# Kernel tuning notes

Hardware: AMD Instinct MI355X
Metric: run time of the kernel (lower is better)

## Reference

```python
import jax, jax.numpy as jnp
import numpy as np

B, T, D, H, HD, FF = 1024, 128, 128, 4, 32, 512
SCALE = D ** -0.5  # NOTE: original scales by full EMBED_DIM**-0.5, not head_dim
EPS = 1e-5


def setup_inputs() -> dict:
    key = jax.random.key(0)
    ks = jax.random.split(key, 14)
    s = 0.02
    return {
        "x": jax.random.normal(ks[0], (B, T, D), dtype=jnp.float32),
        "ln1_g": jnp.ones((D,), jnp.float32),
        "ln1_b": jnp.zeros((D,), jnp.float32),
        "Wq": jax.random.normal(ks[1], (H, HD, D), jnp.float32) * s,
        "Wk": jax.random.normal(ks[2], (H, HD, D), jnp.float32) * s,
        "Wv": jax.random.normal(ks[3], (H, HD, D), jnp.float32) * s,
        "Wo": jax.random.normal(ks[4], (D, D), jnp.float32) * s,
        "bo": jnp.zeros((D,), jnp.float32),
        "ln2_g": jnp.ones((D,), jnp.float32),
        "ln2_b": jnp.zeros((D,), jnp.float32),
        "W1": jax.random.normal(ks[5], (FF, D), jnp.float32) * s,
        "b1": jnp.zeros((FF,), jnp.float32),
        "W2": jax.random.normal(ks[6], (D, FF), jnp.float32) * s,
        "b2": jnp.zeros((D,), jnp.float32),
    }


def _layer_norm(x, g, b):
    mu = jnp.mean(x, axis=-1, keepdims=True)
    var = jnp.mean(jnp.square(x - mu), axis=-1, keepdims=True)
    return (x - mu) * jax.lax.rsqrt(var + EPS) * g + b


def reference(x, ln1_g, ln1_b, Wq, Wk, Wv, Wo, bo, ln2_g, ln2_b, W1, b1, W2, b2):
    # --- attention sub-block ---
    h = _layer_norm(x, ln1_g, ln1_b)                       # [B,T,D]
    q = jnp.einsum('btd,nhd->bnth', h, Wq)                 # [B,H,T,HD]
    k = jnp.einsum('btd,nhd->bnth', h, Wk)
    v = jnp.einsum('btd,nhd->bnth', h, Wv)
    scores = jnp.einsum('bnth,bnsh->bnts', q, k) * SCALE   # [B,H,T,T]
    causal = jnp.tril(jnp.ones((T, T), dtype=bool))
    scores = jnp.where(causal, scores, -jnp.inf)
    w = jax.nn.softmax(scores, axis=-1)                    # dropout = eval identity
    attn = jnp.einsum('bnts,bnsh->bnth', w, v)             # [B,H,T,HD]
    attn = attn.transpose(0, 2, 1, 3).reshape(B, T, D)     # concat heads
    x = x + attn @ Wo.T + bo
    # --- feed-forward sub-block ---
    h2 = _layer_norm(x, ln2_g, ln2_b)
    ff = jax.nn.relu(h2 @ W1.T + b1) @ W2.T + b2
    return x + ff
```

## Files before the change

kernel.cpp:

```cpp
#include <hip/hip_runtime.h>
#include <hip/hip_bf16.h>


typedef short bf16x8 __attribute__((ext_vector_type(8)));
typedef float f32x4  __attribute__((ext_vector_type(4)));
typedef unsigned short u16;
typedef unsigned int   u32;

#define TT   128
#define DDIM 128
#define FFD  512
#define PIT  136

__device__ __forceinline__ u16 f2b(float f) {
    __hip_bfloat16 h = __float2bfloat16(f);
    return __builtin_bit_cast(u16, h);
}
__device__ __forceinline__ bf16x8 ldfrag(const u16* p) {
    return __builtin_bit_cast(bf16x8, *reinterpret_cast<const uint4*>(p));
}
__device__ __forceinline__ bf16x8 ldfrag_f32(const float* p) {
    float4 a = *reinterpret_cast<const float4*>(p);
    float4 b = *reinterpret_cast<const float4*>(p + 4);
    bf16x8 r;
    r[0] = (short)f2b(a.x); r[1] = (short)f2b(a.y);
    r[2] = (short)f2b(a.z); r[3] = (short)f2b(a.w);
    r[4] = (short)f2b(b.x); r[5] = (short)f2b(b.y);
    r[6] = (short)f2b(b.z); r[7] = (short)f2b(b.w);
    return r;
}
__device__ __forceinline__ f32x4 mfma16(bf16x8 a, bf16x8 b, f32x4 c) {
    return __builtin_amdgcn_mfma_f32_16x16x32_bf16(a, b, c, 0, 0, 0);
}

__global__ __launch_bounds__(512, 2) void tblock_kernel(
    const float* __restrict__ x,
    const float* __restrict__ ln1g, const float* __restrict__ ln1b,
    const float* __restrict__ Wq,   const float* __restrict__ Wk, const float* __restrict__ Wv,
    const float* __restrict__ Wo,   const float* __restrict__ bo,
    const float* __restrict__ ln2g, const float* __restrict__ ln2b,
    const float* __restrict__ W1,   const float* __restrict__ b1,
    const float* __restrict__ W2,   const float* __restrict__ b2,
    float* __restrict__ out)
{
    __shared__ __align__(16) u16 sm[4 * TT * PIT];
    u16* bufA = sm;
    u16* bufB = sm + 1 * TT * PIT;
    u16* bufC = sm + 2 * TT * PIT;
    u16* bufD = sm + 3 * TT * PIT;

    const int b    = blockIdx.x;
    const int tid  = threadIdx.x;
    const int w    = tid >> 6;
    const int l    = tid & 63;
    const int lq   = l & 15;
    const int quad = l >> 4;
    const float* xb = x + (size_t)b * (TT * DDIM);

    {
        const int row = tid >> 2, part = tid & 3;
        const float* src = xb + row * DDIM + part * 32;
        float v[32];
        float s = 0.f, s2 = 0.f;
        #pragma unroll
        for (int i = 0; i < 8; i++) {
            float4 u = *reinterpret_cast<const float4*>(src + i * 4);
            v[i * 4 + 0] = u.x; v[i * 4 + 1] = u.y;
            v[i * 4 + 2] = u.z; v[i * 4 + 3] = u.w;
            s  += u.x + u.y + u.z + u.w;
            s2 += u.x * u.x + u.y * u.y + u.z * u.z + u.w * u.w;
        }
        s  += __shfl_xor(s, 1);  s2 += __shfl_xor(s2, 1);
        s  += __shfl_xor(s, 2);  s2 += __shfl_xor(s2, 2);
        float mean = s * (1.f / 128.f);
        float var  = fmaxf(s2 * (1.f / 128.f) - mean * mean, 0.f);
        float rstd = rsqrtf(var + 1e-5f);
        u16* dst = bufA + row * PIT + part * 32;
        #pragma unroll
        for (int i = 0; i < 4; i++) {
            u32 o4[4];
            #pragma unroll
            for (int j = 0; j < 4; j++) {
                int c = part * 32 + i * 8 + 2 * j;
                float r0 = (v[i * 8 + 2 * j]     - mean) * rstd * ln1g[c]     + ln1b[c];
                float r1 = (v[i * 8 + 2 * j + 1] - mean) * rstd * ln1g[c + 1] + ln1b[c + 1];
                o4[j] = (u32)f2b(r0) | ((u32)f2b(r1) << 16);
            }
            uint4 pk; pk.x = o4[0]; pk.y = o4[1]; pk.z = o4[2]; pk.w = o4[3];
            *reinterpret_cast<uint4*>(dst + i * 8) = pk;
        }
    }
    __syncthreads();

    {
        bf16x8 bq[4], bk[4];
        #pragma unroll
        for (int ks = 0; ks < 4; ks++) {
            bq[ks] = ldfrag_f32(Wq + (w * 16 + lq) * DDIM + ks * 32 + quad * 8);
            bk[ks] = ldfrag_f32(Wk + (w * 16 + lq) * DDIM + ks * 32 + quad * 8);
        }
        #pragma unroll
        for (int m = 0; m < 8; m++) {
            f32x4 accq = {0, 0, 0, 0}, acck = {0, 0, 0, 0};
            #pragma unroll
            for (int ks = 0; ks < 4; ks++) {
                bf16x8 a = ldfrag(bufA + (m * 16 + lq) * PIT + ks * 32 + quad * 8);
                accq = mfma16(a, bq[ks], accq);
                acck = mfma16(a, bk[ks], acck);
            }
            #pragma unroll
            for (int r = 0; r < 4; r++) {
                int t = m * 16 + quad * 4 + r;
                bufB[t * PIT + w * 16 + lq] = f2b(accq[r]);
                bufC[t * PIT + w * 16 + lq] = f2b(acck[r]);
            }
        }
        bf16x8 av[4];
        #pragma unroll
        for (int ks = 0; ks < 4; ks++)
            av[ks] = ldfrag_f32(Wv + (w * 16 + lq) * DDIM + ks * 32 + quad * 8);
        #pragma unroll
        for (int n = 0; n < 8; n++) {
            f32x4 acc = {0, 0, 0, 0};
            #pragma unroll
            for (int ks = 0; ks < 4; ks++) {
                bf16x8 bh = ldfrag(bufA + (n * 16 + lq) * PIT + ks * 32 + quad * 8);
                acc = mfma16(av[ks], bh, acc);
            }
            #pragma unroll
            for (int r = 0; r < 4; r++) {
                int o = w * 16 + quad * 4 + r;
                bufD[o * PIT + n * 16 + lq] = f2b(acc[r]);
            }
        }
    }
    __syncthreads();

    const float SCALE = 0.08838834764831845f;
    #pragma unroll 1
    for (int h = 0; h < 4; h++) {
        bf16x8 aq = ldfrag(bufB + (w * 16 + lq) * PIT + h * 32 + quad * 8);
        float p[8][4];
        #pragma unroll
        for (int n = 0; n < 8; n++) {
            bf16x8 bk = ldfrag(bufC + (n * 16 + lq) * PIT + h * 32 + quad * 8);
            f32x4 s4 = {0, 0, 0, 0};
            s4 = mfma16(aq, bk, s4);
            #pragma unroll
            for (int r = 0; r < 4; r++) p[n][r] = s4[r];
        }
        #pragma unroll
        for (int r = 0; r < 4; r++) {
            int t = w * 16 + quad * 4 + r;
            float mx = -3.0e38f;
            #pragma unroll
            for (int n = 0; n < 8; n++) {
                int sc = n * 16 + lq;
                float val = p[n][r] * SCALE;
                p[n][r] = val;
                mx = (sc <= t) ? fmaxf(mx, val) : mx;
            }
            mx = fmaxf(mx, __shfl_xor(mx, 1));
            mx = fmaxf(mx, __shfl_xor(mx, 2));
            mx = fmaxf(mx, __shfl_xor(mx, 4));
            mx = fmaxf(mx, __shfl_xor(mx, 8));
            float sum = 0.f;
            #pragma unroll
            for (int n = 0; n < 8; n++) {
                int sc = n * 16 + lq;
                float e = (sc <= t) ? __expf(p[n][r] - mx) : 0.f;
                p[n][r] = e; sum += e;
            }
            sum += __shfl_xor(sum, 1);
            sum += __shfl_xor(sum, 2);
            sum += __shfl_xor(sum, 4);
            sum += __shfl_xor(sum, 8);
            float inv = 1.f / sum;
            #pragma unroll
            for (int n = 0; n < 8; n++)
                bufA[t * PIT + n * 16 + lq] = f2b(p[n][r] * inv);
        }
        __syncthreads();
        f32x4 o0 = {0, 0, 0, 0}, o1 = {0, 0, 0, 0};
        #pragma unroll
        for (int ks = 0; ks < 4; ks++) {
            bf16x8 ap  = ldfrag(bufA + (w * 16 + lq) * PIT + ks * 32 + quad * 8);
            bf16x8 bv0 = ldfrag(bufD + (h * 32 + lq) * PIT + ks * 32 + quad * 8);
            bf16x8 bv1 = ldfrag(bufD + (h * 32 + 16 + lq) * PIT + ks * 32 + quad * 8);
            o0 = mfma16(ap, bv0, o0);
            o1 = mfma16(ap, bv1, o1);
        }
        __syncthreads();
        #pragma unroll
        for (int r = 0; r < 4; r++) {
            int t = w * 16 + quad * 4 + r;
            bufB[t * PIT + h * 32 + lq]      = f2b(o0[r]);
            bufB[t * PIT + h * 32 + 16 + lq] = f2b(o1[r]);
        }
    }
    __syncthreads();

    float x1res[8][4];
    const int dcol = w * 16 + lq;
    {
        bf16x8 bw[4];
        #pragma unroll
        for (int ks = 0; ks < 4; ks++)
            bw[ks] = ldfrag_f32(Wo + (w * 16 + lq) * DDIM + ks * 32 + quad * 8);
        const float bov = bo[dcol];
        #pragma unroll
        for (int m = 0; m < 8; m++) {
            f32x4 acc = {0, 0, 0, 0};
            #pragma unroll
            for (int ks = 0; ks < 4; ks++) {
                bf16x8 a = ldfrag(bufB + (m * 16 + lq) * PIT + ks * 32 + quad * 8);
                acc = mfma16(a, bw[ks], acc);
            }
            #pragma unroll
            for (int r = 0; r < 4; r++) {
                int t = m * 16 + quad * 4 + r;
                float xv = xb[t * DDIM + dcol];
                float x1 = acc[r] + xv + bov;
                x1res[m][r] = x1;
                bufC[t * PIT + dcol] = f2b(x1);
            }
        }
    }
    __syncthreads();

    {
        const int row = tid >> 2, part = tid & 3;
        const u16* src = bufC + row * PIT + part * 32;
        float v[32];
        float s = 0.f, s2 = 0.f;
        #pragma unroll
        for (int i = 0; i < 4; i++) {
            uint4 u = *reinterpret_cast<const uint4*>(src + i * 8);
            u32 arr[4] = {u.x, u.y, u.z, u.w};
            #pragma unroll
            for (int j = 0; j < 4; j++) {
                float f0 = __uint_as_float((arr[j] & 0xffffu) << 16);
                float f1 = __uint_as_float(arr[j] & 0xffff0000u);
                v[i * 8 + 2 * j] = f0; v[i * 8 + 2 * j + 1] = f1;
                s += f0 + f1; s2 += f0 * f0 + f1 * f1;
            }
        }
        s  += __shfl_xor(s, 1);  s2 += __shfl_xor(s2, 1);
        s  += __shfl_xor(s, 2);  s2 += __shfl_xor(s2, 2);
        float mean = s * (1.f / 128.f);
        float var  = fmaxf(s2 * (1.f / 128.f) - mean * mean, 0.f);
        float rstd = rsqrtf(var + 1e-5f);
        u16* dst = bufD + row * PIT + part * 32;
        #pragma unroll
        for (int i = 0; i < 4; i++) {
            u32 o4[4];
            #pragma unroll
            for (int j = 0; j < 4; j++) {
                int c = part * 32 + i * 8 + 2 * j;
                float r0 = (v[i * 8 + 2 * j]     - mean) * rstd * ln2g[c]     + ln2b[c];
                float r1 = (v[i * 8 + 2 * j + 1] - mean) * rstd * ln2g[c + 1] + ln2b[c + 1];
                o4[j] = (u32)f2b(r0) | ((u32)f2b(r1) << 16);
            }
            uint4 pk; pk.x = o4[0]; pk.y = o4[1]; pk.z = o4[2]; pk.w = o4[3];
            *reinterpret_cast<uint4*>(dst + i * 8) = pk;
        }
    }
    __syncthreads();

    f32x4 oacc[8];
    #pragma unroll
    for (int m = 0; m < 8; m++) oacc[m] = f32x4{0, 0, 0, 0};

    #pragma unroll 1
    for (int fc = 0; fc < 4; fc++) {
        const int fbase = fc * 128;
        bf16x8 wf1[4];
        #pragma unroll
        for (int ks = 0; ks < 4; ks++)
            wf1[ks] = ldfrag_f32(W1 + (fbase + w * 16 + lq) * DDIM + ks * 32 + quad * 8);
        const float b1v = b1[fbase + w * 16 + lq];
        #pragma unroll
        for (int m = 0; m < 8; m++) {
            f32x4 acc = {0, 0, 0, 0};
            #pragma unroll
            for (int ks = 0; ks < 4; ks++) {
                bf16x8 a = ldfrag(bufD + (m * 16 + lq) * PIT + ks * 32 + quad * 8);
                acc = mfma16(a, wf1[ks], acc);
            }
            #pragma unroll
            for (int r = 0; r < 4; r++) {
                int t = m * 16 + quad * 4 + r;
                float g = acc[r] + b1v;
                g = g > 0.f ? g : 0.f;
                bufA[t * PIT + w * 16 + lq] = f2b(g);
            }
        }
        __syncthreads();
        bf16x8 wf2[4];
        #pragma unroll
        for (int ks = 0; ks < 4; ks++)
            wf2[ks] = ldfrag_f32(W2 + (w * 16 + lq) * FFD + fbase + ks * 32 + quad * 8);
        #pragma unroll
        for (int m = 0; m < 8; m++) {
            #pragma unroll
            for (int ks = 0; ks < 4; ks++) {
                bf16x8 a = ldfrag(bufA + (m * 16 + lq) * PIT + ks * 32 + quad * 8);
                oacc[m] = mfma16(a, wf2[ks], oacc[m]);
            }
        }
        __syncthreads();
    }

    {
        const float b2v = b2[dcol];
        float* ob = out + (size_t)b * (TT * DDIM);
        #pragma unroll
        for (int m = 0; m < 8; m++) {
            #pragma unroll
            for (int r = 0; r < 4; r++) {
                int t = m * 16 + quad * 4 + r;
                ob[t * DDIM + dcol] = oacc[m][r] + x1res[m][r] + b2v;
            }
        }
    }
}

extern "C" void kernel_launch(void* const* d_in, const int* in_sizes, int n_in,
                              void* d_out, int out_size, void* d_ws, size_t ws_size,
                              hipStream_t stream) {
    const float* x    = (const float*)d_in[0];
    const float* ln1g = (const float*)d_in[1];
    const float* ln1b = (const float*)d_in[2];
    const float* Wq   = (const float*)d_in[3];
    const float* Wk   = (const float*)d_in[4];
    const float* Wv   = (const float*)d_in[5];
    const float* Wo   = (const float*)d_in[6];
    const float* bo   = (const float*)d_in[7];
    const float* ln2g = (const float*)d_in[8];
    const float* ln2b = (const float*)d_in[9];
    const float* W1   = (const float*)d_in[10];
    const float* b1   = (const float*)d_in[11];
    const float* W2   = (const float*)d_in[12];
    const float* b2   = (const float*)d_in[13];
    float* out = (float*)d_out;

    const int nblocks = in_sizes[0] / (TT * DDIM);
    tblock_kernel<<<dim3(nblocks), dim3(512), 0, stream>>>(
        x, ln1g, ln1b, Wq, Wk, Wv, Wo, bo, ln2g, ln2b, W1, b1, W2, b2, out);
}
```

Measured before the change: 323.3 us.

## Compute QKV per head, fuse Wo per head, and shrink LDS for higher occupancy

Attention is restructured so Q, K and V are computed one head at a time into small per-head LDS buffers, and the Wo projection is accumulated per head in registers. Shared memory drops from four 128x136 buffers to about 74KB, which allows the launch bound to target 4 blocks per CU instead of 2. It also skips causally masked score and PV tiles using the wave-uniform wave index. In exchange there are more barriers per head and more reloads of the weights from global memory, and register pressure rises under the tighter launch bound.

Result: slower. 448.4 us (+38.7%).

```diff
diff --git a/kernel.cpp b/kernel.cpp
--- a/kernel.cpp
+++ b/kernel.cpp
@@ -11,6 +11,7 @@
 #define DDIM 128
 #define FFD  512
 #define PIT  136
+#define QPIT 40
 
 __device__ __forceinline__ u16 f2b(float f) {
     __hip_bfloat16 h = __float2bfloat16(f);
@@ -33,7 +34,7 @@
     return __builtin_amdgcn_mfma_f32_16x16x32_bf16(a, b, c, 0, 0, 0);
 }
 
-__global__ __launch_bounds__(512, 2) void tblock_kernel(
+__global__ __launch_bounds__(512, 4) void tblock_kernel(
     const float* __restrict__ x,
     const float* __restrict__ ln1g, const float* __restrict__ ln1b,
     const float* __restrict__ Wq,   const float* __restrict__ Wk, const float* __restrict__ Wv,
@@ -43,11 +44,13 @@
     const float* __restrict__ W2,   const float* __restrict__ b2,
     float* __restrict__ out)
 {
-    __shared__ __align__(16) u16 sm[4 * TT * PIT];
-    u16* bufA = sm;
-    u16* bufB = sm + 1 * TT * PIT;
-    u16* bufC = sm + 2 * TT * PIT;
-    u16* bufD = sm + 3 * TT * PIT;
+    __shared__ __align__(16) u16 sm[37120];
+    u16* hs  = sm;
+    u16* Qh  = sm + 17408;
+    u16* Kh  = sm + 22528;
+    u16* Vth = sm + 27648;
+    u16* Pst = sm + 32000;
+    u16* h2b = sm + 17408;
 
     const int b    = blockIdx.x;
     const int tid  = threadIdx.x;
@@ -55,7 +58,9 @@
     const int l    = tid & 63;
     const int lq   = l & 15;
     const int quad = l >> 4;
+    const int wu   = __builtin_amdgcn_readfirstlane(w);
     const float* xb = x + (size_t)b * (TT * DDIM);
+    const int dcol = w * 16 + lq;
 
     {
         const int row = tid >> 2, part = tid & 3;
@@ -75,7 +80,7 @@
         float mean = s * (1.f / 128.f);
         float var  = fmaxf(s2 * (1.f / 128.f) - mean * mean, 0.f);
         float rstd = rsqrtf(var + 1e-5f);
-        u16* dst = bufA + row * PIT + part * 32;
+        u16* dst = hs + row * PIT + part * 32;
         #pragma unroll
         for (int i = 0; i < 4; i++) {
             u32 o4[4];
@@ -92,137 +97,148 @@
     }
     __syncthreads();
 
-    {
-        bf16x8 bq[4], bk[4];
-        #pragma unroll
-        for (int ks = 0; ks < 4; ks++) {
-            bq[ks] = ldfrag_f32(Wq + (w * 16 + lq) * DDIM + ks * 32 + quad * 8);
-            bk[ks] = ldfrag_f32(Wk + (w * 16 + lq) * DDIM + ks * 32 + quad * 8);
-        }
-        #pragma unroll
-        for (int m = 0; m < 8; m++) {
-            f32x4 accq = {0, 0, 0, 0}, acck = {0, 0, 0, 0};
-            #pragma unroll
-            for (int ks = 0; ks < 4; ks++) {
-                bf16x8 a = ldfrag(bufA + (m * 16 + lq) * PIT + ks * 32 + quad * 8);
-                accq = mfma16(a, bq[ks], accq);
-                acck = mfma16(a, bk[ks], acck);
-            }
-            #pragma unroll
-            for (int r = 0; r < 4; r++) {
-                int t = m * 16 + quad * 4 + r;
-                bufB[t * PIT + w * 16 + lq] = f2b(accq[r]);
-                bufC[t * PIT + w * 16 + lq] = f2b(acck[r]);
-            }
-        }
-        bf16x8 av[4];
-        #pragma unroll
-        for (int ks = 0; ks < 4; ks++)
-            av[ks] = ldfrag_f32(Wv + (w * 16 + lq) * DDIM + ks * 32 + quad * 8);
-        #pragma unroll
-        for (int n = 0; n < 8; n++) {
-            f32x4 acc = {0, 0, 0, 0};
-            #pragma unroll
-            for (int ks = 0; ks < 4; ks++) {
-                bf16x8 bh = ldfrag(bufA + (n * 16 + lq) * PIT + ks * 32 + quad * 8);
-                acc = mfma16(av[ks], bh, acc);
-            }
-            #pragma unroll
-            for (int r = 0; r < 4; r++) {
-                int o = w * 16 + quad * 4 + r;
-                bufD[o * PIT + n * 16 + lq] = f2b(acc[r]);
-            }
-        }
-    }
-    __syncthreads();
-
     const float SCALE = 0.08838834764831845f;
+    f32x4 x1a[8];
+    #pragma unroll
+    for (int m = 0; m < 8; m++) x1a[m] = f32x4{0, 0, 0, 0};
+
     #pragma unroll 1
     for (int h = 0; h < 4; h++) {
-        bf16x8 aq = ldfrag(bufB + (w * 16 + lq) * PIT + h * 32 + quad * 8);
-        float p[8][4];
-        #pragma unroll
-        for (int n = 0; n < 8; n++) {
-            bf16x8 bk = ldfrag(bufC + (n * 16 + lq) * PIT + h * 32 + quad * 8);
-            f32x4 s4 = {0, 0, 0, 0};
-            s4 = mfma16(aq, bk, s4);
-            #pragma unroll
-            for (int r = 0; r < 4; r++) p[n][r] = s4[r];
-        }
-        #pragma unroll
-        for (int r = 0; r < 4; r++) {
-            int t = w * 16 + quad * 4 + r;
-            float mx = -3.0e38f;
+        {
+            const float* WqB = Wq + (size_t)(h * 32) * DDIM;
+            const float* WkB = Wk + (size_t)(h * 32) * DDIM;
+            #pragma unroll
+            for (int nt = 0; nt < 2; nt++) {
+                f32x4 aq = {0, 0, 0, 0}, ak = {0, 0, 0, 0};
+                #pragma unroll
+                for (int ks = 0; ks < 4; ks++) {
+                    bf16x8 a  = ldfrag(hs + (w * 16 + lq) * PIT + ks * 32 + quad * 8);
+                    bf16x8 bq = ldfrag_f32(WqB + (nt * 16 + lq) * DDIM + ks * 32 + quad * 8);
+                    bf16x8 bk = ldfrag_f32(WkB + (nt * 16 + lq) * DDIM + ks * 32 + quad * 8);
+                    aq = mfma16(a, bq, aq);
+                    ak = mfma16(a, bk, ak);
+                }
+                #pragma unroll
+                for (int r = 0; r < 4; r++) {
+                    int t = w * 16 + quad * 4 + r;
+                    Qh[t * QPIT + nt * 16 + lq] = f2b(aq[r]);
+                    Kh[t * QPIT + nt * 16 + lq] = f2b(ak[r]);
+                }
+            }
+            const float* WvB = Wv + (size_t)(h * 32) * DDIM;
+            #pragma unroll
+            for (int mt = 0; mt < 2; mt++) {
+                f32x4 av = {0, 0, 0, 0};
+                #pragma unroll
+                for (int ks = 0; ks < 4; ks++) {
+                    bf16x8 a  = ldfrag_f32(WvB + (mt * 16 + lq) * DDIM + ks * 32 + quad * 8);
+                    bf16x8 bh = ldfrag(hs + (w * 16 + lq) * PIT + ks * 32 + quad * 8);
+                    av = mfma16(a, bh, av);
+                }
+                #pragma unroll
+                for (int r = 0; r < 4; r++) {
+                    int o = mt * 16 + quad * 4 + r;
+                    Vth[o * PIT + w * 16 + lq] = f2b(av[r]);
+                }
+            }
+        }
+        __syncthreads();
+
+        {
+            bf16x8 aq = ldfrag(Qh + (w * 16 + lq) * QPIT + quad * 8);
+            float p[8][4];
+            #pragma unroll
+            for (int n = 0; n < 8; n++)
+                #pragma unroll
+                for (int r = 0; r < 4; r++) p[n][r] = 0.f;
             #pragma unroll
             for (int n = 0; n < 8; n++) {
-                int sc = n * 16 + lq;
-                float val = p[n][r] * SCALE;
-                p[n][r] = val;
-                mx = (sc <= t) ? fmaxf(mx, val) : mx;
-            }
-            mx = fmaxf(mx, __shfl_xor(mx, 1));
-            mx = fmaxf(mx, __shfl_xor(mx, 2));
-            mx = fmaxf(mx, __shfl_xor(mx, 4));
-            mx = fmaxf(mx, __shfl_xor(mx, 8));
-            float sum = 0.f;
-            #pragma unroll
-            for (int n = 0; n < 8; n++) {
-                int sc = n * 16 + lq;
-                float e = (sc <= t) ? __expf(p[n][r] - mx) : 0.f;
-                p[n][r] = e; sum += e;
-            }
-            sum += __shfl_xor(sum, 1);
-            sum += __shfl_xor(sum, 2);
-            sum += __shfl_xor(sum, 4);
-            sum += __shfl_xor(sum, 8);
-            float inv = 1.f / sum;
-            #pragma unroll
-            for (int n = 0; n < 8; n++)
-                bufA[t * PIT + n * 16 + lq] = f2b(p[n][r] * inv);
+                if (n <= wu) {
+                    bf16x8 bk = ldfrag(Kh + (n * 16 + lq) * QPIT + quad * 8);
+                    f32x4 s4 = {0, 0, 0, 0};
+                    s4 = mfma16(aq, bk, s4);
+                    #pragma unroll
+                    for (int r = 0; r < 4; r++) p[n][r] = s4[r];
+                }
+            }
+            #pragma unroll
+            for (int r = 0; r < 4; r++) {
+                int t = w * 16 + quad * 4 + r;
+                float mx = -3.0e38f;
+                #pragma unroll
+                for (int n = 0; n < 8; n++) {
+                    int sc = n * 16 + lq;
+                    float val = p[n][r] * SCALE;
+                    p[n][r] = val;
+                    mx = (sc <= t) ? fmaxf(mx, val) : mx;
+                }
+                mx = fmaxf(mx, __shfl_xor(mx, 1));
+                mx = fmaxf(mx, __shfl_xor(mx, 2));
+                mx = fmaxf(mx, __shfl_xor(mx, 4));
+                mx = fmaxf(mx, __shfl_xor(mx, 8));
+                float sum = 0.f;
+                #pragma unroll
+                for (int n = 0; n < 8; n++) {
+                    int sc = n * 16 + lq;
+                    float e = (sc <= t) ? __expf(p[n][r] - mx) : 0.f;
+                    p[n][r] = e; sum += e;
+                }
+                sum += __shfl_xor(sum, 1);
+                sum += __shfl_xor(sum, 2);
+                sum += __shfl_xor(sum, 4);
+                sum += __shfl_xor(sum, 8);
+                float inv = 1.f / sum;
+                #pragma unroll
+                for (int n = 0; n < 8; n++) p[n][r] *= inv;
+            }
+            f32x4 o0 = {0, 0, 0, 0}, o1 = {0, 0, 0, 0};
+            #pragma unroll
+            for (int s = 0; s < 4; s++) {
+                if (s <= (wu >> 1)) {
+                    #pragma unroll
+                    for (int r = 0; r < 4; r++) {
+                        int t = w * 16 + quad * 4 + r;
+                        Pst[t * QPIT + lq]      = f2b(p[2 * s][r]);
+                        Pst[t * QPIT + 16 + lq] = f2b(p[2 * s + 1][r]);
+                    }
+                    bf16x8 ap  = ldfrag(Pst + (w * 16 + lq) * QPIT + quad * 8);
+                    bf16x8 bv0 = ldfrag(Vth + lq * PIT        + s * 32 + quad * 8);
+                    bf16x8 bv1 = ldfrag(Vth + (16 + lq) * PIT + s * 32 + quad * 8);
+                    o0 = mfma16(ap, bv0, o0);
+                    o1 = mfma16(ap, bv1, o1);
+                }
+            }
+            #pragma unroll
+            for (int r = 0; r < 4; r++) {
+                int t = w * 16 + quad * 4 + r;
+                Qh[t * QPIT + lq]      = f2b(o0[r]);
+                Qh[t * QPIT + 16 + lq] = f2b(o1[r]);
+            }
         }
         __syncthreads();
-        f32x4 o0 = {0, 0, 0, 0}, o1 = {0, 0, 0, 0};
-        #pragma unroll
-        for (int ks = 0; ks < 4; ks++) {
-            bf16x8 ap  = ldfrag(bufA + (w * 16 + lq) * PIT + ks * 32 + quad * 8);
-            bf16x8 bv0 = ldfrag(bufD + (h * 32 + lq) * PIT + ks * 32 + quad * 8);
-            bf16x8 bv1 = ldfrag(bufD + (h * 32 + 16 + lq) * PIT + ks * 32 + quad * 8);
-            o0 = mfma16(ap, bv0, o0);
-            o1 = mfma16(ap, bv1, o1);
-        }
-        __syncthreads();
-        #pragma unroll
-        for (int r = 0; r < 4; r++) {
-            int t = w * 16 + quad * 4 + r;
-            bufB[t * PIT + h * 32 + lq]      = f2b(o0[r]);
-            bufB[t * PIT + h * 32 + 16 + lq] = f2b(o1[r]);
-        }
-    }
-    __syncthreads();
-
-    float x1res[8][4];
-    const int dcol = w * 16 + lq;
+
+        {
+            bf16x8 bwo = ldfrag_f32(Wo + (size_t)(w * 16 + lq) * DDIM + h * 32 + quad * 8);
+            #pragma unroll
+            for (int m = 0; m < 8; m++) {
+                bf16x8 a = ldfrag(Qh + (m * 16 + lq) * QPIT + quad * 8);
+                x1a[m] = mfma16(a, bwo, x1a[m]);
+            }
+        }
+        if (h < 3) __syncthreads();
+    }
+
     {
-        bf16x8 bw[4];
-        #pragma unroll
-        for (int ks = 0; ks < 4; ks++)
-            bw[ks] = ldfrag_f32(Wo + (w * 16 + lq) * DDIM + ks * 32 + quad * 8);
         const float bov = bo[dcol];
         #pragma unroll
         for (int m = 0; m < 8; m++) {
-            f32x4 acc = {0, 0, 0, 0};
-            #pragma unroll
-            for (int ks = 0; ks < 4; ks++) {
-                bf16x8 a = ldfrag(bufB + (m * 16 + lq) * PIT + ks * 32 + quad * 8);
-                acc = mfma16(a, bw[ks], acc);
-            }
             #pragma unroll
             for (int r = 0; r < 4; r++) {
                 int t = m * 16 + quad * 4 + r;
                 float xv = xb[t * DDIM + dcol];
-                float x1 = acc[r] + xv + bov;
-                x1res[m][r] = x1;
-                bufC[t * PIT + dcol] = f2b(x1);
+                float v = x1a[m][r] + xv + bov;
+                x1a[m][r] = v;
+                hs[t * PIT + dcol] = f2b(v);
             }
         }
     }
@@ -230,7 +246,7 @@
 
     {
         const int row = tid >> 2, part = tid & 3;
-        const u16* src = bufC + row * PIT + part * 32;
+        const u16* src = hs + row * PIT + part * 32;
         float v[32];
         float s = 0.f, s2 = 0.f;
         #pragma unroll
@@ -250,7 +266,7 @@
         float mean = s * (1.f / 128.f);
         float var  = fmaxf(s2 * (1.f / 128.f) - mean * mean, 0.f);
         float rstd = rsqrtf(var + 1e-5f);
-        u16* dst = bufD + row * PIT + part * 32;
+        u16* dst = h2b + row * PIT + part * 32;
         #pragma unroll
         for (int i = 0; i < 4; i++) {
             u32 o4[4];
@@ -270,6 +286,7 @@
     f32x4 oacc[8];
     #pragma unroll
     for (int m = 0; m < 8; m++) oacc[m] = f32x4{0, 0, 0, 0};
+    u16* Gb = hs;
 
     #pragma unroll 1
     for (int fc = 0; fc < 4; fc++) {
@@ -277,14 +294,14 @@
         bf16x8 wf1[4];
         #pragma unroll
         for (int ks = 0; ks < 4; ks++)
-            wf1[ks] = ldfrag_f32(W1 + (fbase + w * 16 + lq) * DDIM + ks * 32 + quad * 8);
+            wf1[ks] = ldfrag_f32(W1 + (size_t)(fbase + w * 16 + lq) * DDIM + ks * 32 + quad * 8);
         const float b1v = b1[fbase + w * 16 + lq];
         #pragma unroll
         for (int m = 0; m < 8; m++) {
             f32x4 acc = {0, 0, 0, 0};
             #pragma unroll
             for (int ks = 0; ks < 4; ks++) {
-                bf16x8 a = ldfrag(bufD + (m * 16 + lq) * PIT + ks * 32 + quad * 8);
+                bf16x8 a = ldfrag(h2b + (m * 16 + lq) * PIT + ks * 32 + quad * 8);
                 acc = mfma16(a, wf1[ks], acc);
             }
             #pragma unroll
@@ -292,19 +309,19 @@
                 int t = m * 16 + quad * 4 + r;
                 float g = acc[r] + b1v;
                 g = g > 0.f ? g : 0.f;
-                bufA[t * PIT + w * 16 + lq] = f2b(g);
+                Gb[t * PIT + w * 16 + lq] = f2b(g);
             }
         }
         __syncthreads();
         bf16x8 wf2[4];
         #pragma unroll
         for (int ks = 0; ks < 4; ks++)
-            wf2[ks] = ldfrag_f32(W2 + (w * 16 + lq) * FFD + fbase + ks * 32 + quad * 8);
+            wf2[ks] = ldfrag_f32(W2 + (size_t)(w * 16 + lq) * FFD + fbase + ks * 32 + quad * 8);
         #pragma unroll
         for (int m = 0; m < 8; m++) {
             #pragma unroll
             for (int ks = 0; ks < 4; ks++) {
-                bf16x8 a = ldfrag(bufA + (m * 16 + lq) * PIT + ks * 32 + quad * 8);
+                bf16x8 a = ldfrag(Gb + (m * 16 + lq) * PIT + ks * 32 + quad * 8);
                 oacc[m] = mfma16(a, wf2[ks], oacc[m]);
             }
         }
@@ -319,7 +336,7 @@
             #pragma unroll
             for (int r = 0; r < 4; r++) {
                 int t = m * 16 + quad * 4 + r;
-                ob[t * DDIM + dcol] = oacc[m][r] + x1res[m][r] + b2v;
+                ob[t * DDIM + dcol] = oacc[m][r] + x1a[m][r] + b2v;
             }
         }
     }
```
